# Performance work log

Hardware: AMD Instinct MI355X
Metric: run time of the kernel (lower is better)

The kernel has to match this reference:

```python
import jax, jax.numpy as jnp
import numpy as np
from jax.scipy.special import logsumexp

N, K, D = 131072, 256, 32


def setup_inputs() -> dict:
    key = jax.random.key(0)
    k1, k2, k3 = jax.random.split(key, 3)
    points = jax.random.normal(k1, (N, D), dtype=jnp.float32)
    centers = jax.random.uniform(k2, (K, D), dtype=jnp.float32)
    # well-conditioned inverse-sqrt covariances (original used 15*I; scaled to
    # avoid float32 overflow in sqrt(det(covs_inv)) for D=32)
    covs_inv_sqrt = (0.5 * jnp.broadcast_to(jnp.eye(D, dtype=jnp.float32), (K, D, D))
                     + 0.02 * jax.random.normal(k3, (K, D, D), dtype=jnp.float32))
    weights = jnp.ones((K,), dtype=jnp.float32)
    threshold = jnp.zeros((1,), dtype=jnp.float32)
    return {"points": points, "centers": centers,
            "covs_inv_sqrt": covs_inv_sqrt, "weights": weights,
            "threshold": threshold}


def reference(points, centers, covs_inv_sqrt, weights, threshold):
    # refresh(): equal_clusters=True branch
    w = jnp.abs(weights)
    center_prs = w / (w.sum() + 1e-30)                       # [K]
    covs_inv = jnp.einsum('kde,kfe->kdf', covs_inv_sqrt, covs_inv_sqrt)  # [K,D,D]
    coefs = center_prs * jnp.sqrt(jnp.linalg.det(covs_inv))  # [K]

    # pairwise weighted sqdist: q_ij = (x_i - c_j)^T A_j (x_i - c_j)
    B = covs_inv.reshape(K, D * D)                           # [K, D*D]
    X2 = (points[:, :, None] * points[:, None, :]).reshape(N, D * D)  # [N, D*D]
    t_xAx = X2 @ B.T                                         # [N, K]
    m = jnp.einsum('kde,ke->kd', covs_inv, centers)          # A_j c_j, [K,D]
    t_xAc = points @ m.T                                     # [N, K]
    t_cAc = jnp.einsum('kd,kd->k', m, centers)               # [K]
    d_ij = -0.5 * (t_xAx - 2.0 * t_xAc + t_cAc[None, :])     # [N, K]

    # weighted logsumexp over centers, then subtract threshold
    ll = logsumexp(d_ij, axis=1, b=coefs[None, :])           # [N]
    return ll[:, None] - threshold[0]                        # [N, 1]
```

## Files before the change

### kernel.cpp

```cpp
#include <hip/hip_runtime.h>
#include <hip/hip_fp16.h>
#include <math.h>

#define NPTS 131072
#define KCOMP 256
#define DIM 32
#define KF 608
#define PSIF_BYTES 311296
#define WS_NEED (PSIF_BYTES + KCOMP * 4)

typedef _Float16 f16x8 __attribute__((ext_vector_type(8)));
typedef __attribute__((ext_vector_type(16))) float f32x16;

constexpr int L4c(int d) { return ((32 - d + 3) / 4) * 4; }
constexpr int PfxC(int d) { int s = 0; for (int i = 0; i < d; ++i) s += L4c(i); return s; }
constexpr int rowOfC(int p) { int d = 0; while (d < 31 && PfxC(d + 1) <= p) ++d; return d; }
constexpr int dOfC(int p) { return (p >= 576) ? -1 : rowOfC(p); }
constexpr int f0OfC(int p) {
    return (p >= 576) ? (p - 576) : ((rowOfC(p) & ~3) + (p - PfxC(rowOfC(p))));
}

__device__ __forceinline__ unsigned short f2h(float v) {
    __half h = __float2half(v);
    return __builtin_bit_cast(unsigned short, h);
}

__device__ __forceinline__ void barrier_lds_only() {
    asm volatile("s_waitcnt lgkmcnt(0)\ns_barrier" ::: "memory");
}

__global__ __launch_bounds__(256) void gmm_pre(
    const float* __restrict__ S,
    const float* __restrict__ centers,
    const float* __restrict__ weights,
    unsigned short* __restrict__ PsiF,
    float* __restrict__ kc2)
{
    __shared__ float Sl[DIM][DIM + 1];
    __shared__ float As[DIM][DIM + 1];
    __shared__ float cl[DIM], ml[DIM];
    __shared__ float red[256];

    const int k = blockIdx.x, tid = threadIdx.x;

    for (int idx = tid; idx < DIM * DIM; idx += 256)
        Sl[idx >> 5][idx & 31] = S[(size_t)k * DIM * DIM + idx];
    if (tid < DIM) cl[tid] = centers[k * DIM + tid];
    __syncthreads();

    for (int idx = tid; idx < DIM * DIM; idx += 256) {
        const int d = idx >> 5, f = idx & 31;
        float a = 0.f;
#pragma unroll
        for (int e = 0; e < DIM; ++e) a = fmaf(Sl[d][e], Sl[f][e], a);
        As[d][f] = a;
    }
    __syncthreads();

    if (tid < DIM) {
        float mv = 0.f;
#pragma unroll
        for (int f = 0; f < DIM; ++f) mv = fmaf(As[tid][f], cl[f], mv);
        ml[tid] = mv;
    }
    __syncthreads();

    for (int p = tid; p < KF; p += 256) {
        float val;
        if (p < 576) {
            int d = 0, pr = 0;
            while (true) {
                const int len = ((32 - d + 3) >> 2) << 2;
                if (pr + len > p) break;
                pr += len; ++d;
            }
            const int f = (d & ~3) + (p - pr);
            val = (f < d) ? 0.f : ((f == d) ? -0.5f * As[d][d] : -As[d][f]);
        } else {
            val = ml[p - 576];
        }
        const int c = p >> 6, kk = p & 63;
        const int s = kk >> 4, qq = (kk >> 3) & 1, j = kk & 7;
        const int ct = k >> 5, ll = qq * 32 + (k & 31);
        const int g = c * 2048 + (s * 8 + ct) * 64 + ll;
        PsiF[(size_t)g * 8 + j] = f2h(val);
    }

    red[tid] = fabsf(weights[tid]);
    __syncthreads();
    for (int off = 128; off > 0; off >>= 1) {
        if (tid < off) red[tid] += red[tid + off];
        __syncthreads();
    }
    const float wsum = red[0];

    for (int j = 0; j < DIM - 1; ++j) {
        const float inv = 1.0f / As[j][j];
        for (int idx = tid; idx < DIM * DIM; idx += 256) {
            const int r = idx >> 5, c = idx & 31;
            if (r > j && c > j)
                As[r][c] = fmaf(-As[r][j] * inv, As[j][c], As[r][c]);
        }
        __syncthreads();
    }

    if (tid < DIM) red[tid] = __logf(As[tid][tid]);
    __syncthreads();
    if (tid == 0) {
        float sl = 0.f;
        for (int j = 0; j < DIM; ++j) sl += red[j];
        float cac = 0.f;
        for (int d2 = 0; d2 < DIM; ++d2) cac = fmaf(ml[d2], cl[d2], cac);
        kc2[k] = __logf(fabsf(weights[k])) - __logf(wsum + 1e-30f)
               + 0.5f * sl - 0.5f * cac;
    }
}

__device__ __forceinline__ unsigned pkmul(unsigned a, unsigned b) {
    __half2 r = __builtin_bit_cast(__half2, a) * __builtin_bit_cast(__half2, b);
    return __builtin_bit_cast(unsigned, r);
}

template<int P>
__device__ __forceinline__ void genQuadH(const unsigned (&xp)[16],
                                         unsigned& o0, unsigned& o1) {
    constexpr int d = dOfC(P);
    constexpr int f0 = f0OfC(P);
    const unsigned p0 = xp[(f0 >> 1) + 0];
    const unsigned p1 = xp[(f0 >> 1) + 1];
    if constexpr (d < 0) { o0 = p0; o1 = p1; }
    else {
        const unsigned ss = __builtin_amdgcn_perm(xp[d >> 1], xp[d >> 1],
                                (d & 1) ? 0x03020302u : 0x01000100u);
        o0 = pkmul(ss, p0); o1 = pkmul(ss, p1);
    }
}

template<int C, int SS>
__device__ __forceinline__ void genSiteH(const unsigned (&xp)[16],
                                         uint4* buf, int row) {
    uint4 u;
    genQuadH<C * 64 + SS * 8>(xp, u.x, u.y);
    genQuadH<C * 64 + SS * 8 + 4>(xp, u.z, u.w);
    buf[(SS >> 1) * 128 + (row >> 5) * 64 + (SS & 1) * 32 + (row & 31)] = u;
}

template<int ST>
__device__ __forceinline__ void doStep(
    const uint4* buf, uint4 (&bf)[4][2], f32x16 (&acc)[2][2],
    const uint4* __restrict__ pb, int l)
{
    constexpr int S = (ST < 36) ? ST % 4 : ST - 36;

    if constexpr (ST + 3 <= 37) {
#pragma unroll
        for (int ct = 0; ct < 2; ++ct)
            bf[(ST + 3) & 3][ct] = pb[(ST + 3) * 512 + ct * 64];
    }

    const f16x8 a0 = __builtin_bit_cast(f16x8, buf[S * 128 + 0 * 64 + l]);
    const f16x8 a1 = __builtin_bit_cast(f16x8, buf[S * 128 + 1 * 64 + l]);
#pragma unroll
    for (int ct = 0; ct < 2; ++ct) {
        const f16x8 b = __builtin_bit_cast(f16x8, bf[ST & 3][ct]);
        acc[0][ct] = __builtin_amdgcn_mfma_f32_32x32x16_f16(a0, b, acc[0][ct], 0, 0, 0);
        acc[1][ct] = __builtin_amdgcn_mfma_f32_32x32x16_f16(a1, b, acc[1][ct], 0, 0, 0);
    }
}

template<int C>
__device__ __forceinline__ void doChunk(
    const unsigned (&xp)[16], uint4* sA4,
    uint4 (&bf)[4][2], f32x16 (&acc)[2][2],
    const uint4* __restrict__ pb, int l, int sub, int row)
{
    constexpr int NS = (C < 9) ? 4 : 2;
    uint4* buf = sA4 + (C & 1) * 512;

    if constexpr (NS == 4) {
        switch (sub) {
        case 0: genSiteH<C, 0>(xp, buf, row); genSiteH<C, 4>(xp, buf, row); break;
        case 1: genSiteH<C, 1>(xp, buf, row); genSiteH<C, 5>(xp, buf, row); break;
        case 2: genSiteH<C, 2>(xp, buf, row); genSiteH<C, 6>(xp, buf, row); break;
        default: genSiteH<C, 3>(xp, buf, row); genSiteH<C, 7>(xp, buf, row); break;
        }
    } else {
        switch (sub) {
        case 0: genSiteH<C, 0>(xp, buf, row); break;
        case 1: genSiteH<C, 1>(xp, buf, row); break;
        case 2: genSiteH<C, 2>(xp, buf, row); break;
        default: genSiteH<C, 3>(xp, buf, row); break;
        }
    }
    barrier_lds_only();

    doStep<C * 4 + 0>(buf, bf, acc, pb, l);
    doStep<C * 4 + 1>(buf, bf, acc, pb, l);
    if constexpr (NS == 4) {
        doStep<C * 4 + 2>(buf, bf, acc, pb, l);
        doStep<C * 4 + 3>(buf, bf, acc, pb, l);
    }
}

__global__ __launch_bounds__(256, 3) void gmm_mfma(
    const float* __restrict__ points,
    const unsigned short* __restrict__ PsiF,
    const float* __restrict__ kc2,
    const float* __restrict__ thr,
    float* __restrict__ out)
{
    __shared__ uint4 sA4[1024];
    __shared__ float sPm[64][4], sPs[64][4];

    const int t = threadIdx.x;
    const int cq = t >> 6, l = t & 63;
    const int row = l;

    const uint4* pb = (const uint4*)PsiF + cq * 128 + l;

    unsigned xp[16];
    {
        const float4* px = (const float4*)(points + ((size_t)blockIdx.x * 64 + row) * DIM);
#pragma unroll
        for (int i = 0; i < 8; ++i) {
            float4 v = px[i];
            xp[2 * i + 0] = __builtin_bit_cast(unsigned, __floats2half2_rn(v.x, v.y));
            xp[2 * i + 1] = __builtin_bit_cast(unsigned, __floats2half2_rn(v.z, v.w));
        }
    }

    uint4 bf[4][2];
#pragma unroll
    for (int st = 0; st < 3; ++st)
#pragma unroll
        for (int ct = 0; ct < 2; ++ct)
            bf[st][ct] = pb[st * 512 + ct * 64];

    f32x16 acc[2][2];
#pragma unroll
    for (int a = 0; a < 2; ++a)
#pragma unroll
        for (int c = 0; c < 2; ++c)
#pragma unroll
            for (int r = 0; r < 16; ++r) acc[a][c][r] = 0.f;

    doChunk<0>(xp, sA4, bf, acc, pb, l, cq, row);
    doChunk<1>(xp, sA4, bf, acc, pb, l, cq, row);
    doChunk<2>(xp, sA4, bf, acc, pb, l, cq, row);
    doChunk<3>(xp, sA4, bf, acc, pb, l, cq, row);
    doChunk<4>(xp, sA4, bf, acc, pb, l, cq, row);
    doChunk<5>(xp, sA4, bf, acc, pb, l, cq, row);
    doChunk<6>(xp, sA4, bf, acc, pb, l, cq, row);
    doChunk<7>(xp, sA4, bf, acc, pb, l, cq, row);
    doChunk<8>(xp, sA4, bf, acc, pb, l, cq, row);
    doChunk<9>(xp, sA4, bf, acc, pb, l, cq, row);

    float kcv[2];
#pragma unroll
    for (int ct = 0; ct < 2; ++ct) kcv[ct] = kc2[(cq * 2 + ct) * 32 + (l & 31)];

#pragma unroll
    for (int rt = 0; rt < 2; ++rt) {
#pragma unroll
        for (int rg = 0; rg < 16; ++rg) {
            const float v0 = acc[rt][0][rg] + kcv[0];
            const float v1 = acc[rt][1][rg] + kcv[1];
            float m = fmaxf(v0, v1);
#pragma unroll
            for (int mask = 1; mask < 32; mask <<= 1)
                m = fmaxf(m, __shfl_xor(m, mask, 64));
            float sv = __expf(v0 - m) + __expf(v1 - m);
#pragma unroll
            for (int mask = 1; mask < 32; mask <<= 1)
                sv += __shfl_xor(sv, mask, 64);
            if ((l & 31) == 0) {
                const int R = rt * 32 + (rg & 3) + 8 * (rg >> 2) + 4 * (l >> 5);
                sPm[R][cq] = m; sPs[R][cq] = sv;
            }
        }
    }
    __syncthreads();

    if (t < 64) {
        const float m0 = sPm[t][0], m1 = sPm[t][1];
        const float m2 = sPm[t][2], m3 = sPm[t][3];
        const float M = fmaxf(fmaxf(m0, m1), fmaxf(m2, m3));
        const float Sv = sPs[t][0] * __expf(m0 - M) + sPs[t][1] * __expf(m1 - M)
                       + sPs[t][2] * __expf(m2 - M) + sPs[t][3] * __expf(m3 - M);
        out[(size_t)blockIdx.x * 64 + t] = M + __logf(Sv) - thr[0];
    }
}

extern "C" void kernel_launch(void* const* d_in, const int* in_sizes, int n_in,
                              void* d_out, int out_size, void* d_ws, size_t ws_size,
                              hipStream_t stream) {
    const float* points  = (const float*)d_in[0];
    const float* centers = (const float*)d_in[1];
    const float* covs    = (const float*)d_in[2];
    const float* weights = (const float*)d_in[3];
    const float* thr     = (const float*)d_in[4];
    float* out = (float*)d_out;

    unsigned short* PsiF = (unsigned short*)d_ws;
    float* kc2 = (float*)((char*)d_ws + PSIF_BYTES);

    gmm_pre<<<KCOMP, 256, 0, stream>>>(covs, centers, weights, PsiF, kc2);
    gmm_mfma<<<NPTS / 64, 256, 0, stream>>>(points, PsiF, kc2, thr, out);
}
```

Baseline: 152.6 us.

## Use LDS point rows and descriptor table with rolled double-buffered B prefetch

```diff
diff --git a/kernel.cpp b/kernel.cpp
--- a/kernel.cpp
+++ b/kernel.cpp
@@ -7,18 +7,12 @@
 #define DIM 32
 #define KF 608
 #define PSIF_BYTES 311296
-#define WS_NEED (PSIF_BYTES + KCOMP * 4)
+#define KC2_BYTES 1024
+#define TAB_OFF (PSIF_BYTES + KC2_BYTES)
+#define WS_NEED (TAB_OFF + 320)
 
 typedef _Float16 f16x8 __attribute__((ext_vector_type(8)));
 typedef __attribute__((ext_vector_type(16))) float f32x16;
-
-constexpr int L4c(int d) { return ((32 - d + 3) / 4) * 4; }
-constexpr int PfxC(int d) { int s = 0; for (int i = 0; i < d; ++i) s += L4c(i); return s; }
-constexpr int rowOfC(int p) { int d = 0; while (d < 31 && PfxC(d + 1) <= p) ++d; return d; }
-constexpr int dOfC(int p) { return (p >= 576) ? -1 : rowOfC(p); }
-constexpr int f0OfC(int p) {
-    return (p >= 576) ? (p - 576) : ((rowOfC(p) & ~3) + (p - PfxC(rowOfC(p))));
-}
 
 __device__ __forceinline__ unsigned short f2h(float v) {
     __half h = __float2half(v);
@@ -27,6 +21,11 @@
 
 __device__ __forceinline__ void barrier_lds_only() {
     asm volatile("s_waitcnt lgkmcnt(0)\ns_barrier" ::: "memory");
+}
+
+__device__ __forceinline__ unsigned pkmul(unsigned a, unsigned b) {
+    __half2 r = __builtin_bit_cast(__half2, a) * __builtin_bit_cast(__half2, b);
+    return __builtin_bit_cast(unsigned, r);
 }
 
 __global__ __launch_bounds__(256) void gmm_pre(
@@ -34,7 +33,8 @@
     const float* __restrict__ centers,
     const float* __restrict__ weights,
     unsigned short* __restrict__ PsiF,
-    float* __restrict__ kc2)
+    float* __restrict__ kc2,
+    unsigned* __restrict__ gTab)
 {
     __shared__ float Sl[DIM][DIM + 1];
     __shared__ float As[DIM][DIM + 1];
@@ -42,6 +42,27 @@
     __shared__ float red[256];
 
     const int k = blockIdx.x, tid = threadIdx.x;
+
+    if (k == 0 && tid < 80) {
+        unsigned desc = 0;
+        for (int qi = 0; qi < 2; ++qi) {
+            const int p = (tid >> 3) * 64 + (tid & 7) * 8 + qi * 4;
+            unsigned d, f;
+            if (p >= 576) { d = 255u; f = (unsigned)(p - 576); }
+            else {
+                int dd = 0, pr = 0;
+                while (true) {
+                    const int len = ((32 - dd + 3) >> 2) << 2;
+                    if (pr + len > p) break;
+                    pr += len; ++dd;
+                }
+                d = (unsigned)dd;
+                f = (unsigned)((dd & ~3) + (p - pr));
+            }
+            desc |= (d | (f << 8)) << (qi * 16);
+        }
+        gTab[tid] = desc;
+    }
 
     for (int idx = tid; idx < DIM * DIM; idx += 256)
         Sl[idx >> 5][idx & 31] = S[(size_t)k * DIM * DIM + idx];
@@ -116,125 +137,100 @@
     }
 }
 
-__device__ __forceinline__ unsigned pkmul(unsigned a, unsigned b) {
-    __half2 r = __builtin_bit_cast(__half2, a) * __builtin_bit_cast(__half2, b);
-    return __builtin_bit_cast(unsigned, r);
-}
-
-template<int P>
-__device__ __forceinline__ void genQuadH(const unsigned (&xp)[16],
-                                         unsigned& o0, unsigned& o1) {
-    constexpr int d = dOfC(P);
-    constexpr int f0 = f0OfC(P);
-    const unsigned p0 = xp[(f0 >> 1) + 0];
-    const unsigned p1 = xp[(f0 >> 1) + 1];
-    if constexpr (d < 0) { o0 = p0; o1 = p1; }
-    else {
-        const unsigned ss = __builtin_amdgcn_perm(xp[d >> 1], xp[d >> 1],
-                                (d & 1) ? 0x03020302u : 0x01000100u);
-        o0 = pkmul(ss, p0); o1 = pkmul(ss, p1);
-    }
-}
-
-template<int C, int SS>
-__device__ __forceinline__ void genSiteH(const unsigned (&xp)[16],
-                                         uint4* buf, int row) {
+__device__ __forceinline__ void quadR(const unsigned short* sx, int rowb,
+                                      unsigned d, unsigned f0,
+                                      unsigned& o0, unsigned& o1) {
+    const bool mk = (d == 255u);
+    const unsigned short* rp =
+        (const unsigned short*)((const char*)sx + rowb);
+    const unsigned xdu = rp[d & 31u];
+    const uint2 xf = *(const uint2*)((const char*)sx + rowb + f0 * 2u);
+    const unsigned sd = __builtin_amdgcn_perm(xdu, xdu, 0x01000100u);
+    o0 = mk ? xf.x : pkmul(sd, xf.x);
+    o1 = mk ? xf.y : pkmul(sd, xf.y);
+}
+
+__device__ __forceinline__ void genSiteR(const unsigned short* sx, int rowb,
+                                         unsigned desc, uint4* buf,
+                                         int row, int SS) {
     uint4 u;
-    genQuadH<C * 64 + SS * 8>(xp, u.x, u.y);
-    genQuadH<C * 64 + SS * 8 + 4>(xp, u.z, u.w);
+    quadR(sx, rowb, desc & 255u, (desc >> 8) & 255u, u.x, u.y);
+    quadR(sx, rowb, (desc >> 16) & 255u, desc >> 24, u.z, u.w);
     buf[(SS >> 1) * 128 + (row >> 5) * 64 + (SS & 1) * 32 + (row & 31)] = u;
 }
 
-template<int ST>
-__device__ __forceinline__ void doStep(
-    const uint4* buf, uint4 (&bf)[4][2], f32x16 (&acc)[2][2],
-    const uint4* __restrict__ pb, int l)
-{
-    constexpr int S = (ST < 36) ? ST % 4 : ST - 36;
-
-    if constexpr (ST + 3 <= 37) {
+__device__ __forceinline__ void genChunk(const unsigned short* sx, int rowb,
+                                         const unsigned* sTab, int c, int cq,
+                                         uint4* buf, int row, bool full) {
+    genSiteR(sx, rowb, sTab[c * 8 + cq], buf, row, cq);
+    if (full) genSiteR(sx, rowb, sTab[c * 8 + cq + 4], buf, row, cq + 4);
+}
+
+__device__ __forceinline__ void issueB(uint4 (&bf)[8], const uint4* pc) {
+#pragma unroll
+    for (int s = 0; s < 4; ++s)
 #pragma unroll
         for (int ct = 0; ct < 2; ++ct)
-            bf[(ST + 3) & 3][ct] = pb[(ST + 3) * 512 + ct * 64];
-    }
-
-    const f16x8 a0 = __builtin_bit_cast(f16x8, buf[S * 128 + 0 * 64 + l]);
-    const f16x8 a1 = __builtin_bit_cast(f16x8, buf[S * 128 + 1 * 64 + l]);
+            bf[s * 2 + ct] = pc[s * 512 + ct * 64];
+}
+
+template<int S>
+__device__ __forceinline__ void stepR(const uint4* buf, const uint4 (&bf)[8],
+                                      f32x16 (&acc)[2][2], int l) {
+    const f16x8 a0 = __builtin_bit_cast(f16x8, buf[S * 128 + l]);
+    const f16x8 a1 = __builtin_bit_cast(f16x8, buf[S * 128 + 64 + l]);
 #pragma unroll
     for (int ct = 0; ct < 2; ++ct) {
-        const f16x8 b = __builtin_bit_cast(f16x8, bf[ST & 3][ct]);
+        const f16x8 b = __builtin_bit_cast(f16x8, bf[S * 2 + ct]);
         acc[0][ct] = __builtin_amdgcn_mfma_f32_32x32x16_f16(a0, b, acc[0][ct], 0, 0, 0);
         acc[1][ct] = __builtin_amdgcn_mfma_f32_32x32x16_f16(a1, b, acc[1][ct], 0, 0, 0);
     }
 }
 
-template<int C>
-__device__ __forceinline__ void doChunk(
-    const unsigned (&xp)[16], uint4* sA4,
-    uint4 (&bf)[4][2], f32x16 (&acc)[2][2],
-    const uint4* __restrict__ pb, int l, int sub, int row)
-{
-    constexpr int NS = (C < 9) ? 4 : 2;
-    uint4* buf = sA4 + (C & 1) * 512;
-
-    if constexpr (NS == 4) {
-        switch (sub) {
-        case 0: genSiteH<C, 0>(xp, buf, row); genSiteH<C, 4>(xp, buf, row); break;
-        case 1: genSiteH<C, 1>(xp, buf, row); genSiteH<C, 5>(xp, buf, row); break;
-        case 2: genSiteH<C, 2>(xp, buf, row); genSiteH<C, 6>(xp, buf, row); break;
-        default: genSiteH<C, 3>(xp, buf, row); genSiteH<C, 7>(xp, buf, row); break;
-        }
-    } else {
-        switch (sub) {
-        case 0: genSiteH<C, 0>(xp, buf, row); break;
-        case 1: genSiteH<C, 1>(xp, buf, row); break;
-        case 2: genSiteH<C, 2>(xp, buf, row); break;
-        default: genSiteH<C, 3>(xp, buf, row); break;
-        }
-    }
-    barrier_lds_only();
-
-    doStep<C * 4 + 0>(buf, bf, acc, pb, l);
-    doStep<C * 4 + 1>(buf, bf, acc, pb, l);
-    if constexpr (NS == 4) {
-        doStep<C * 4 + 2>(buf, bf, acc, pb, l);
-        doStep<C * 4 + 3>(buf, bf, acc, pb, l);
-    }
-}
-
-__global__ __launch_bounds__(256, 3) void gmm_mfma(
+__device__ __forceinline__ void mfma4(const uint4* buf, const uint4 (&bf)[8],
+                                      f32x16 (&acc)[2][2], int l) {
+    stepR<0>(buf, bf, acc, l); stepR<1>(buf, bf, acc, l);
+    stepR<2>(buf, bf, acc, l); stepR<3>(buf, bf, acc, l);
+}
+
+__global__ __launch_bounds__(256, 2) void gmm_mfma(
     const float* __restrict__ points,
     const unsigned short* __restrict__ PsiF,
     const float* __restrict__ kc2,
+    const unsigned* __restrict__ gTab,
     const float* __restrict__ thr,
     float* __restrict__ out)
 {
+    __shared__ unsigned short sxp[64 * 36];
     __shared__ uint4 sA4[1024];
+    __shared__ unsigned sTab[80];
     __shared__ float sPm[64][4], sPs[64][4];
 
     const int t = threadIdx.x;
     const int cq = t >> 6, l = t & 63;
     const int row = l;
+    const int rowb = row * 72;
+
+    {
+        const int rr = t & 63, q = t >> 6;
+        const float4* px = (const float4*)(points +
+            ((size_t)blockIdx.x * 64 + rr) * DIM + q * 8);
+        const float4 v0 = px[0], v1 = px[1];
+        uint2 w0, w1;
+        w0.x = __builtin_bit_cast(unsigned, __floats2half2_rn(v0.x, v0.y));
+        w0.y = __builtin_bit_cast(unsigned, __floats2half2_rn(v0.z, v0.w));
+        w1.x = __builtin_bit_cast(unsigned, __floats2half2_rn(v1.x, v1.y));
+        w1.y = __builtin_bit_cast(unsigned, __floats2half2_rn(v1.z, v1.w));
+        *(uint2*)((char*)sxp + rr * 72 + q * 16) = w0;
+        *(uint2*)((char*)sxp + rr * 72 + q * 16 + 8) = w1;
+    }
+    if (t < 80) sTab[t] = gTab[t];
+    __syncthreads();
 
     const uint4* pb = (const uint4*)PsiF + cq * 128 + l;
 
-    unsigned xp[16];
-    {
-        const float4* px = (const float4*)(points + ((size_t)blockIdx.x * 64 + row) * DIM);
-#pragma unroll
-        for (int i = 0; i < 8; ++i) {
-            float4 v = px[i];
-            xp[2 * i + 0] = __builtin_bit_cast(unsigned, __floats2half2_rn(v.x, v.y));
-            xp[2 * i + 1] = __builtin_bit_cast(unsigned, __floats2half2_rn(v.z, v.w));
-        }
-    }
-
-    uint4 bf[4][2];
-#pragma unroll
-    for (int st = 0; st < 3; ++st)
-#pragma unroll
-        for (int ct = 0; ct < 2; ++ct)
-            bf[st][ct] = pb[st * 512 + ct * 64];
+    uint4 bfA[8], bfB[8];
+    issueB(bfA, pb);
 
     f32x16 acc[2][2];
 #pragma unroll
@@ -244,16 +240,27 @@
 #pragma unroll
             for (int r = 0; r < 16; ++r) acc[a][c][r] = 0.f;
 
-    doChunk<0>(xp, sA4, bf, acc, pb, l, cq, row);
-    doChunk<1>(xp, sA4, bf, acc, pb, l, cq, row);
-    doChunk<2>(xp, sA4, bf, acc, pb, l, cq, row);
-    doChunk<3>(xp, sA4, bf, acc, pb, l, cq, row);
-    doChunk<4>(xp, sA4, bf, acc, pb, l, cq, row);
-    doChunk<5>(xp, sA4, bf, acc, pb, l, cq, row);
-    doChunk<6>(xp, sA4, bf, acc, pb, l, cq, row);
-    doChunk<7>(xp, sA4, bf, acc, pb, l, cq, row);
-    doChunk<8>(xp, sA4, bf, acc, pb, l, cq, row);
-    doChunk<9>(xp, sA4, bf, acc, pb, l, cq, row);
+    const uint4* pn = pb + 2048;
+
+#pragma unroll 1
+    for (int i = 0; i < 4; ++i) {
+        genChunk(sxp, rowb, sTab, 2 * i, cq, sA4, row, true);
+        issueB(bfB, pn); pn += 2048;
+        barrier_lds_only();
+        mfma4(sA4, bfA, acc, l);
+        genChunk(sxp, rowb, sTab, 2 * i + 1, cq, sA4 + 512, row, true);
+        issueB(bfA, pn); pn += 2048;
+        barrier_lds_only();
+        mfma4(sA4 + 512, bfB, acc, l);
+    }
+    genChunk(sxp, rowb, sTab, 8, cq, sA4, row, true);
+    issueB(bfB, pn);
+    barrier_lds_only();
+    mfma4(sA4, bfA, acc, l);
+    genChunk(sxp, rowb, sTab, 9, cq, sA4 + 512, row, false);
+    barrier_lds_only();
+    stepR<0>(sA4 + 512, bfB, acc, l);
+    stepR<1>(sA4 + 512, bfB, acc, l);
 
     float kcv[2];
 #pragma unroll
@@ -303,7 +310,8 @@
 
     unsigned short* PsiF = (unsigned short*)d_ws;
     float* kc2 = (float*)((char*)d_ws + PSIF_BYTES);
-
-    gmm_pre<<<KCOMP, 256, 0, stream>>>(covs, centers, weights, PsiF, kc2);
-    gmm_mfma<<<NPTS / 64, 256, 0, stream>>>(points, PsiF, kc2, thr, out);
-}
+    unsigned* gTab = (unsigned*)((char*)d_ws + TAB_OFF);
+
+    gmm_pre<<<KCOMP, 256, 0, stream>>>(covs, centers, weights, PsiF, kc2, gTab);
+    gmm_mfma<<<NPTS / 64, 256, 0, stream>>>(points, PsiF, kc2, gTab, thr, out);
+}
```

After: 164.3 us. +7.7%, slower.
